# Performance work log

Measured on AMD Instinct MI355X. Metric: run time of the kernel, lower is better.

## Reference

```python
import jax, jax.numpy as jnp
import numpy as np

F = 16        # num_frames
K = 8         # num_tokens (top-k)
SIZE = 64     # basis size
PD = 256      # prompt_dim
ED = 768      # embed_dim
EPS = 1e-12

def _l2norm(v, axis=-1):
    n = jnp.sqrt(jnp.sum(v * v, axis=axis, keepdims=True))
    return v / jnp.maximum(n, EPS)

def setup_inputs() -> dict:
    key = jax.random.key(0)
    k1, k2, k3, k4 = jax.random.split(key, 4)
    B, N = 32, 197
    x = jax.random.normal(k1, (B, F * N, ED), dtype=jnp.float32)
    # prompt_values ~ U(-1, 1), shape [size, 1, prompt_dim]
    prompt_values = jax.random.uniform(k2, (SIZE, 1, PD), dtype=jnp.float32, minval=-1.0, maxval=1.0)
    # prompt_inproj: Linear(embed_dim, prompt_dim, bias=False)
    W_in = jax.random.normal(k3, (PD, ED), dtype=jnp.float32) * (1.0 / np.sqrt(ED))
    # prompt_outproj: Linear(prompt_dim, embed_dim, bias=False), kaiming fan_out
    W_out = jax.random.normal(k4, (ED, PD), dtype=jnp.float32) * np.sqrt(2.0 / ED)
    return {"x": x, "W_in": W_in, "W_out": W_out, "prompt_values": prompt_values}

def reference(x, W_in, W_out, prompt_values):
    B = x.shape[0]
    x = jax.lax.stop_gradient(x)                       # x.detach()
    xf = x.reshape(B, F, -1, ED).mean(axis=2)          # [B, F, ED]
    query = jnp.einsum('bfe,pe->bfp', xf, W_in)        # prompt_inproj
    BZ = B * F
    q = _l2norm(query.reshape(BZ, PD), axis=1)         # [BZ, PD]
    keys = _l2norm(prompt_values.mean(axis=1), axis=1) # [SIZE, PD]
    sim = q @ keys.T                                   # [BZ, SIZE]
    # eval routing: top-k by similarity (argsort descending [:, :k])
    _, idx = jax.lax.top_k(sim, K)                     # [BZ, K] int32
    prompts = prompt_values[idx.reshape(-1)].reshape(BZ, K, PD)
    prompts = _l2norm(prompts, axis=-1)
    sel_sim = jnp.take_along_axis(sim, idx, axis=1)    # [BZ, K]
    sel_key = keys[idx]                                # [BZ, K, PD]
    recon = jnp.einsum('bk,bkd->bd', sel_sim, sel_key) # [BZ, PD]
    diff = jnp.sum((recon - jax.lax.stop_gradient(q)) ** 2) / BZ
    ksim = jnp.sum(jnp.abs(keys @ keys.T - jnp.eye(SIZE, dtype=keys.dtype))) / BZ
    ps = diff + ksim
    # rearrange '(b f) p d -> b (f p) d' then outproj
    out_prompts = prompts.reshape(B, F * K, PD)
    out_prompts = jnp.einsum('bnd,ed->bne', out_prompts, W_out)  # [B, F*K, ED]
    ps_loss = jnp.zeros((1,), dtype=x.dtype) + ps * F
    return out_prompts, ps_loss
```

## Files before the change

### kernel.cpp

```cpp
#include <hip/hip_runtime.h>

#define Ff 16
#define Kk 8
#define SIZEk 64
#define PDd 256
#define EDd 768
#define Nn 197
#define BZz 512
#define ED4 192
#define PD4 64
#define OUT_LOSS ((size_t)32 * 128 * EDd)
#define LOSS_SCALE (1.0f / 32.0f)

__global__ __launch_bounds__(192) void k_mean(const float4* __restrict__ x,
                                              float* __restrict__ xf,
                                              float* __restrict__ out) {
    int bf = blockIdx.x;
    int t  = threadIdx.x;
    if (bf == 0 && t == 0) out[OUT_LOSS] = 0.0f;

    const float4* base = x + (size_t)bf * Nn * ED4;
    float4 s = make_float4(0.f, 0.f, 0.f, 0.f);
    int n = 0;
    for (; n + 4 <= Nn; n += 4) {
        float4 a = base[(n + 0) * ED4 + t];
        float4 b = base[(n + 1) * ED4 + t];
        float4 c = base[(n + 2) * ED4 + t];
        float4 d = base[(n + 3) * ED4 + t];
        s.x += a.x + b.x + c.x + d.x;
        s.y += a.y + b.y + c.y + d.y;
        s.z += a.z + b.z + c.z + d.z;
        s.w += a.w + b.w + c.w + d.w;
    }
    for (; n < Nn; n++) {
        float4 a = base[n * ED4 + t];
        s.x += a.x; s.y += a.y; s.z += a.z; s.w += a.w;
    }
    const float inv = 1.0f / (float)Nn;
    s.x *= inv; s.y *= inv; s.z *= inv; s.w *= inv;
    ((float4*)xf)[(size_t)bf * ED4 + t] = s;
}

__global__ __launch_bounds__(256) void k_query(const float* __restrict__ xf,
                                               const float* __restrict__ Win,
                                               float* __restrict__ q) {
    __shared__ float xs[4][EDd];
    __shared__ float red[4][4];
    __shared__ float norms[4];
    int t   = threadIdx.x;
    int bf0 = blockIdx.x * 4;

    for (int i = t; i < 4 * EDd; i += 256) ((float*)xs)[i] = xf[(size_t)bf0 * EDd + i];
    __syncthreads();

    const float4* w = (const float4*)Win + (size_t)t * ED4;
    float d0 = 0.f, d1 = 0.f, d2 = 0.f, d3 = 0.f;
    for (int i = 0; i < ED4; i++) {
        float4 wv = w[i];
        float4 x0 = ((const float4*)xs[0])[i];
        float4 x1 = ((const float4*)xs[1])[i];
        float4 x2 = ((const float4*)xs[2])[i];
        float4 x3 = ((const float4*)xs[3])[i];
        d0 += wv.x * x0.x + wv.y * x0.y + wv.z * x0.z + wv.w * x0.w;
        d1 += wv.x * x1.x + wv.y * x1.y + wv.z * x1.z + wv.w * x1.w;
        d2 += wv.x * x2.x + wv.y * x2.y + wv.z * x2.z + wv.w * x2.w;
        d3 += wv.x * x3.x + wv.y * x3.y + wv.z * x3.z + wv.w * x3.w;
    }
    float s0 = d0 * d0, s1 = d1 * d1, s2 = d2 * d2, s3 = d3 * d3;
    for (int o = 32; o > 0; o >>= 1) {
        s0 += __shfl_down(s0, o);
        s1 += __shfl_down(s1, o);
        s2 += __shfl_down(s2, o);
        s3 += __shfl_down(s3, o);
    }
    int wid = t >> 6;
    if ((t & 63) == 0) { red[0][wid] = s0; red[1][wid] = s1; red[2][wid] = s2; red[3][wid] = s3; }
    __syncthreads();
    if (t < 4) {
        float ss = red[t][0] + red[t][1] + red[t][2] + red[t][3];
        norms[t] = fmaxf(sqrtf(ss), 1e-12f);
    }
    __syncthreads();
    q[(size_t)(bf0 + 0) * PDd + t] = d0 / norms[0];
    q[(size_t)(bf0 + 1) * PDd + t] = d1 / norms[1];
    q[(size_t)(bf0 + 2) * PDd + t] = d2 / norms[2];
    q[(size_t)(bf0 + 3) * PDd + t] = d3 / norms[3];
}

__global__ __launch_bounds__(256) void k_keys(const float* __restrict__ pv,
                                              const float* __restrict__ Wout,
                                              float* __restrict__ keys,
                                              float* __restrict__ KW) {
    __shared__ float ks[PDd];
    __shared__ float red[4];
    __shared__ float s_norm;
    int s = blockIdx.x, t = threadIdx.x;
    float v  = pv[(size_t)s * PDd + t];
    float sq = v * v;
    for (int o = 32; o > 0; o >>= 1) sq += __shfl_down(sq, o);
    if ((t & 63) == 0) red[t >> 6] = sq;
    __syncthreads();
    if (t == 0) s_norm = fmaxf(sqrtf(red[0] + red[1] + red[2] + red[3]), 1e-12f);
    __syncthreads();
    float kv = v / s_norm;
    ks[t] = kv;
    keys[(size_t)s * PDd + t] = kv;
    __syncthreads();

    for (int e = t; e < EDd; e += 256) {
        const float4* w  = (const float4*)(Wout + (size_t)e * PDd);
        const float4* k4 = (const float4*)ks;
        float d = 0.f;
        for (int i = 0; i < PD4; i++) {
            float4 wv = w[i]; float4 kvv = k4[i];
            d += wv.x * kvv.x + wv.y * kvv.y + wv.z * kvv.z + wv.w * kvv.w;
        }
        KW[(size_t)s * EDd + e] = d;
    }
}

__global__ __launch_bounds__(256) void k_route(const float* __restrict__ q,
                                               const float* __restrict__ keys,
                                               const float* __restrict__ KW,
                                               float* __restrict__ out) {
    int blk = blockIdx.x, t = threadIdx.x;

    if (blk >= BZz) {
        int i = blk - BZz;
        if (t < SIZEk) {
            const float4* a = (const float4*)(keys + (size_t)i * PDd);
            const float4* b = (const float4*)(keys + (size_t)t * PDd);
            float d = 0.f;
            for (int c = 0; c < PD4; c++) {
                float4 av = a[c], bv = b[c];
                d += av.x * bv.x + av.y * bv.y + av.z * bv.z + av.w * bv.w;
            }
            float v = fabsf(d - (i == t ? 1.0f : 0.0f));
            for (int o = 32; o > 0; o >>= 1) v += __shfl_down(v, o);
            if (t == 0) atomicAdd(out + OUT_LOSS, v * LOSS_SCALE);
        }
        return;
    }

    __shared__ float qs[PDd];
    __shared__ int   s_idx[Kk];
    __shared__ float s_sim[Kk];
    __shared__ float red[4];
    int bz = blk;
    qs[t] = q[(size_t)bz * PDd + t];
    __syncthreads();

    if (t < SIZEk) {
        const float4* kr = (const float4*)(keys + (size_t)t * PDd);
        const float4* qr = (const float4*)qs;
        float d = 0.f;
        for (int c = 0; c < PD4; c++) {
            float4 a = kr[c], b = qr[c];
            d += a.x * b.x + a.y * b.y + a.z * b.z + a.w * b.w;
        }
        float v = d;
        for (int k = 0; k < Kk; k++) {
            float mv = v; int mi = t;
            for (int o = 32; o > 0; o >>= 1) {
                float ov = __shfl_xor(mv, o);
                int   oi = __shfl_xor(mi, o);
                if (ov > mv || (ov == mv && oi < mi)) { mv = ov; mi = oi; }
            }
            if (t == 0) { s_idx[k] = mi; s_sim[k] = mv; }
            if (t == mi) v = -3e38f;
        }
    }
    __syncthreads();

    float r = 0.f;
    for (int k = 0; k < Kk; k++) r += s_sim[k] * keys[(size_t)s_idx[k] * PDd + t];
    float e  = r - qs[t];
    float sq = e * e;
    for (int o = 32; o > 0; o >>= 1) sq += __shfl_down(sq, o);
    if ((t & 63) == 0) red[t >> 6] = sq;
    __syncthreads();
    if (t == 0) atomicAdd(out + OUT_LOSS, (red[0] + red[1] + red[2] + red[3]) * LOSS_SCALE);

    float4* orow = (float4*)out + (size_t)bz * Kk * ED4;
    for (int i = t; i < Kk * ED4; i += 256) {
        int k  = i / ED4;
        int e4 = i - k * ED4;
        orow[i] = ((const float4*)(KW + (size_t)s_idx[k] * EDd))[e4];
    }
}

extern "C" void kernel_launch(void* const* d_in, const int* in_sizes, int n_in,
                              void* d_out, int out_size, void* d_ws, size_t ws_size,
                              hipStream_t stream) {
    const float* x    = (const float*)d_in[0];
    const float* Win  = (const float*)d_in[1];
    const float* Wout = (const float*)d_in[2];
    const float* pv   = (const float*)d_in[3];
    float* out = (float*)d_out;
    float* ws  = (float*)d_ws;

    float* xf   = ws;
    float* q    = ws + 393216;
    float* keys = ws + 524288;
    float* KW   = ws + 540672;

    k_mean <<<BZz, 192, 0, stream>>>((const float4*)x, xf, out);
    k_query<<<BZz / 4, 256, 0, stream>>>(xf, Win, q);
    k_keys <<<SIZEk, 256, 0, stream>>>(pv, Wout, keys, KW);
    k_route<<<BZz + SIZEk, 256, 0, stream>>>(q, keys, KW, out);
}
```

Baseline: 514.1 us.

## Fuse frame mean, query projection and routing into a single kernel

Merges the per-frame mean, the W_in projection with L2 normalisation, and the routing/top-k into one kernel, with one block per (batch, frame) row. This removes two launches and the global round-trips for the xf and q intermediates. The mean loop is unrolled by 8 to put more loads in flight. In exchange, each block now reads W_in alone instead of sharing it across 4 rows, which raises L2 traffic, and only 192 of 256 threads take part in the mean phase.

```diff
diff --git a/kernel.cpp b/kernel.cpp
--- a/kernel.cpp
+++ b/kernel.cpp
@@ -12,89 +12,16 @@
 #define OUT_LOSS ((size_t)32 * 128 * EDd)
 #define LOSS_SCALE (1.0f / 32.0f)
 
-__global__ __launch_bounds__(192) void k_mean(const float4* __restrict__ x,
-                                              float* __restrict__ xf,
-                                              float* __restrict__ out) {
-    int bf = blockIdx.x;
-    int t  = threadIdx.x;
-    if (bf == 0 && t == 0) out[OUT_LOSS] = 0.0f;
-
-    const float4* base = x + (size_t)bf * Nn * ED4;
-    float4 s = make_float4(0.f, 0.f, 0.f, 0.f);
-    int n = 0;
-    for (; n + 4 <= Nn; n += 4) {
-        float4 a = base[(n + 0) * ED4 + t];
-        float4 b = base[(n + 1) * ED4 + t];
-        float4 c = base[(n + 2) * ED4 + t];
-        float4 d = base[(n + 3) * ED4 + t];
-        s.x += a.x + b.x + c.x + d.x;
-        s.y += a.y + b.y + c.y + d.y;
-        s.z += a.z + b.z + c.z + d.z;
-        s.w += a.w + b.w + c.w + d.w;
-    }
-    for (; n < Nn; n++) {
-        float4 a = base[n * ED4 + t];
-        s.x += a.x; s.y += a.y; s.z += a.z; s.w += a.w;
-    }
-    const float inv = 1.0f / (float)Nn;
-    s.x *= inv; s.y *= inv; s.z *= inv; s.w *= inv;
-    ((float4*)xf)[(size_t)bf * ED4 + t] = s;
-}
-
-__global__ __launch_bounds__(256) void k_query(const float* __restrict__ xf,
-                                               const float* __restrict__ Win,
-                                               float* __restrict__ q) {
-    __shared__ float xs[4][EDd];
-    __shared__ float red[4][4];
-    __shared__ float norms[4];
-    int t   = threadIdx.x;
-    int bf0 = blockIdx.x * 4;
-
-    for (int i = t; i < 4 * EDd; i += 256) ((float*)xs)[i] = xf[(size_t)bf0 * EDd + i];
-    __syncthreads();
-
-    const float4* w = (const float4*)Win + (size_t)t * ED4;
-    float d0 = 0.f, d1 = 0.f, d2 = 0.f, d3 = 0.f;
-    for (int i = 0; i < ED4; i++) {
-        float4 wv = w[i];
-        float4 x0 = ((const float4*)xs[0])[i];
-        float4 x1 = ((const float4*)xs[1])[i];
-        float4 x2 = ((const float4*)xs[2])[i];
-        float4 x3 = ((const float4*)xs[3])[i];
-        d0 += wv.x * x0.x + wv.y * x0.y + wv.z * x0.z + wv.w * x0.w;
-        d1 += wv.x * x1.x + wv.y * x1.y + wv.z * x1.z + wv.w * x1.w;
-        d2 += wv.x * x2.x + wv.y * x2.y + wv.z * x2.z + wv.w * x2.w;
-        d3 += wv.x * x3.x + wv.y * x3.y + wv.z * x3.z + wv.w * x3.w;
-    }
-    float s0 = d0 * d0, s1 = d1 * d1, s2 = d2 * d2, s3 = d3 * d3;
-    for (int o = 32; o > 0; o >>= 1) {
-        s0 += __shfl_down(s0, o);
-        s1 += __shfl_down(s1, o);
-        s2 += __shfl_down(s2, o);
-        s3 += __shfl_down(s3, o);
-    }
-    int wid = t >> 6;
-    if ((t & 63) == 0) { red[0][wid] = s0; red[1][wid] = s1; red[2][wid] = s2; red[3][wid] = s3; }
-    __syncthreads();
-    if (t < 4) {
-        float ss = red[t][0] + red[t][1] + red[t][2] + red[t][3];
-        norms[t] = fmaxf(sqrtf(ss), 1e-12f);
-    }
-    __syncthreads();
-    q[(size_t)(bf0 + 0) * PDd + t] = d0 / norms[0];
-    q[(size_t)(bf0 + 1) * PDd + t] = d1 / norms[1];
-    q[(size_t)(bf0 + 2) * PDd + t] = d2 / norms[2];
-    q[(size_t)(bf0 + 3) * PDd + t] = d3 / norms[3];
-}
-
 __global__ __launch_bounds__(256) void k_keys(const float* __restrict__ pv,
                                               const float* __restrict__ Wout,
                                               float* __restrict__ keys,
-                                              float* __restrict__ KW) {
+                                              float* __restrict__ KW,
+                                              float* __restrict__ out) {
     __shared__ float ks[PDd];
     __shared__ float red[4];
     __shared__ float s_norm;
     int s = blockIdx.x, t = threadIdx.x;
+    if (s == 0 && t == 0) out[OUT_LOSS] = 0.0f;
     float v  = pv[(size_t)s * PDd + t];
     float sq = v * v;
     for (int o = 32; o > 0; o >>= 1) sq += __shfl_down(sq, o);
@@ -119,7 +46,8 @@
     }
 }
 
-__global__ __launch_bounds__(256) void k_route(const float* __restrict__ q,
+__global__ __launch_bounds__(256) void k_fused(const float4* __restrict__ x,
+                                               const float* __restrict__ Win,
                                                const float* __restrict__ keys,
                                                const float* __restrict__ KW,
                                                float* __restrict__ out) {
@@ -142,12 +70,56 @@
         return;
     }
 
+    __shared__ float xs[EDd];
     __shared__ float qs[PDd];
     __shared__ int   s_idx[Kk];
     __shared__ float s_sim[Kk];
     __shared__ float red[4];
     int bz = blk;
-    qs[t] = q[(size_t)bz * PDd + t];
+
+    if (t < ED4) {
+        const float4* base = x + (size_t)bz * Nn * ED4;
+        float4 s = make_float4(0.f, 0.f, 0.f, 0.f);
+        int n = 0;
+        for (; n + 8 <= Nn; n += 8) {
+            float4 a0 = base[(n + 0) * ED4 + t];
+            float4 a1 = base[(n + 1) * ED4 + t];
+            float4 a2 = base[(n + 2) * ED4 + t];
+            float4 a3 = base[(n + 3) * ED4 + t];
+            float4 a4 = base[(n + 4) * ED4 + t];
+            float4 a5 = base[(n + 5) * ED4 + t];
+            float4 a6 = base[(n + 6) * ED4 + t];
+            float4 a7 = base[(n + 7) * ED4 + t];
+            s.x += ((a0.x + a1.x) + (a2.x + a3.x)) + ((a4.x + a5.x) + (a6.x + a7.x));
+            s.y += ((a0.y + a1.y) + (a2.y + a3.y)) + ((a4.y + a5.y) + (a6.y + a7.y));
+            s.z += ((a0.z + a1.z) + (a2.z + a3.z)) + ((a4.z + a5.z) + (a6.z + a7.z));
+            s.w += ((a0.w + a1.w) + (a2.w + a3.w)) + ((a4.w + a5.w) + (a6.w + a7.w));
+        }
+        for (; n < Nn; n++) {
+            float4 a = base[n * ED4 + t];
+            s.x += a.x; s.y += a.y; s.z += a.z; s.w += a.w;
+        }
+        const float inv = 1.0f / (float)Nn;
+        s.x *= inv; s.y *= inv; s.z *= inv; s.w *= inv;
+        ((float4*)xs)[t] = s;
+    }
+    __syncthreads();
+
+    {
+        const float4* w  = (const float4*)Win + (size_t)t * ED4;
+        const float4* xv = (const float4*)xs;
+        float d = 0.f;
+        for (int i = 0; i < ED4; i++) {
+            float4 wv = w[i], x0 = xv[i];
+            d += wv.x * x0.x + wv.y * x0.y + wv.z * x0.z + wv.w * x0.w;
+        }
+        float sq = d * d;
+        for (int o = 32; o > 0; o >>= 1) sq += __shfl_down(sq, o);
+        if ((t & 63) == 0) red[t >> 6] = sq;
+        __syncthreads();
+        float nrm = fmaxf(sqrtf(red[0] + red[1] + red[2] + red[3]), 1e-12f);
+        qs[t] = d / nrm;
+    }
     __syncthreads();
 
     if (t < SIZEk) {
@@ -172,14 +144,16 @@
     }
     __syncthreads();
 
-    float r = 0.f;
-    for (int k = 0; k < Kk; k++) r += s_sim[k] * keys[(size_t)s_idx[k] * PDd + t];
-    float e  = r - qs[t];
-    float sq = e * e;
-    for (int o = 32; o > 0; o >>= 1) sq += __shfl_down(sq, o);
-    if ((t & 63) == 0) red[t >> 6] = sq;
-    __syncthreads();
-    if (t == 0) atomicAdd(out + OUT_LOSS, (red[0] + red[1] + red[2] + red[3]) * LOSS_SCALE);
+    {
+        float r = 0.f;
+        for (int k = 0; k < Kk; k++) r += s_sim[k] * keys[(size_t)s_idx[k] * PDd + t];
+        float e  = r - qs[t];
+        float sq = e * e;
+        for (int o = 32; o > 0; o >>= 1) sq += __shfl_down(sq, o);
+        if ((t & 63) == 0) red[t >> 6] = sq;
+        __syncthreads();
+        if (t == 0) atomicAdd(out + OUT_LOSS, (red[0] + red[1] + red[2] + red[3]) * LOSS_SCALE);
+    }
 
     float4* orow = (float4*)out + (size_t)bz * Kk * ED4;
     for (int i = t; i < Kk * ED4; i += 256) {
@@ -199,13 +173,9 @@
     float* out = (float*)d_out;
     float* ws  = (float*)d_ws;
 
-    float* xf   = ws;
-    float* q    = ws + 393216;
-    float* keys = ws + 524288;
-    float* KW   = ws + 540672;
+    float* keys = ws;
+    float* KW   = ws + 16384;
 
-    k_mean <<<BZz, 192, 0, stream>>>((const float4*)x, xf, out);
-    k_query<<<BZz / 4, 256, 0, stream>>>(xf, Win, q);
-    k_keys <<<SIZEk, 256, 0, stream>>>(pv, Wout, keys, KW);
-    k_route<<<BZz + SIZEk, 256, 0, stream>>>(q, keys, KW, out);
+    k_keys <<<SIZEk, 256, 0, stream>>>(pv, Wout, keys, KW, out);
+    k_fused<<<BZz + SIZEk, 256, 0, stream>>>((const float4*)x, Win, keys, KW, out);
 }
```

Result: faster. 503.7 us (-2.0%).
